# Optimization experiments

Measured on AMD Instinct MI355X. Metric: run time of the kernel, lower is better.

Reference implementation:

```python
import jax, jax.numpy as jnp
import numpy as np

N = 400000      # total tree nodes (forest batched together)
D = 256         # input feature dim
H = 128         # hidden_dim
C = 16          # num_classes (len(tag_dict))


def setup_inputs() -> dict:
    key = jax.random.key(0)
    ks = jax.random.split(key, 8)
    features = jax.random.normal(ks[0], (N, D), dtype=jnp.float32)
    # parent index per node; force parent[i] < i (topological order), root=0 self-parent
    raw = jax.random.randint(ks[1], (N,), 0, N)
    idx = jnp.arange(N)
    parent = jnp.where(idx == 0, 0, raw % jnp.maximum(idx, 1))
    init = lambda k, shp, fan: (jax.random.normal(k, shp, dtype=jnp.float32) / np.float32(np.sqrt(fan)))
    W1 = init(ks[2], (D, H), D); b1 = jnp.zeros((H,), jnp.float32)
    W2 = init(ks[3], (H, H), H); b2 = jnp.zeros((H,), jnp.float32)
    Wu = init(ks[4], (H, C), H); bu = jnp.zeros((C,), jnp.float32)
    We = init(ks[5], (2 * H, C * C), 2 * H); be = jnp.zeros((C * C,), jnp.float32)
    return {"features": features, "parent": parent,
            "W1": W1, "b1": b1, "W2": W2, "b2": b2,
            "Wu": Wu, "bu": bu, "We": We, "be": be}


def reference(features, parent, W1, b1, W2, b2, Wu, bu, We, be):
    # MLP feature extractor (num_layers=2, outputs hidden_dim)
    h = jax.nn.relu(features @ W1 + b1)          # [N, H]
    h = jax.nn.relu(h @ W2 + b2)                 # [N, H]
    # unary potentials per node
    unary = h @ Wu + bu                          # [N, C]
    # edge potentials per (parent, child) pair: cat(parent_hidden, child_hidden)
    edge_in = jnp.concatenate([h[parent], h], axis=1)   # [N, 2H] irregular gather
    edge = edge_in @ We + be                     # [N, C*C]
    # pack unary + edge potentials into a single output tensor
    return jnp.concatenate([unary, edge], axis=1)       # [N, C + C*C]
```

## Files before the change

### kernel.cpp

```cpp
#include <hip/hip_runtime.h>
#include <hip/hip_bf16.h>

typedef __bf16 bf16x8 __attribute__((ext_vector_type(8)));
typedef float  f32x4  __attribute__((ext_vector_type(4)));

#define MFMA16 __builtin_amdgcn_mfma_f32_16x16x32_bf16

__global__ void shuffle_weights(const float* __restrict__ W, __bf16* __restrict__ out,
                                int K, int Nw) {
    int tid = blockIdx.x * 256 + threadIdx.x;
    int NT = Nw >> 4;
    int total = (K >> 5) * NT * 64;
    if (tid >= total) return;
    int lane = tid & 63;
    int rest = tid >> 6;
    int nt = rest % NT;
    int kc = rest / NT;
    int q = lane >> 4;
    int n = nt * 16 + (lane & 15);
    const float* src = W + (size_t)(kc * 32 + q * 8) * Nw + n;
    __bf16* dst = out + (size_t)tid * 8;
#pragma unroll
    for (int j = 0; j < 8; ++j) dst[j] = (__bf16)src[(size_t)j * Nw];
}

__global__ __launch_bounds__(256) void phase1(
    const float* __restrict__ feat,
    const __bf16* __restrict__ W1s, const float* __restrict__ b1,
    const __bf16* __restrict__ W2s, const float* __restrict__ b2,
    __bf16* __restrict__ hbuf)
{
    __shared__ __bf16 h1s[128 * 136];
    const int lane = threadIdx.x & 63;
    const int wave = threadIdx.x >> 6;
    const int q    = lane >> 4;
    const int mr   = lane & 15;
    const long base = (long)blockIdx.x * 128 + wave * 32;

    const f32x4 fz = {0.f, 0.f, 0.f, 0.f};

    f32x4 acc[2][8];
#pragma unroll
    for (int mt = 0; mt < 2; ++mt)
#pragma unroll
        for (int nt = 0; nt < 8; ++nt) acc[mt][nt] = fz;

#pragma unroll
    for (int kc = 0; kc < 8; ++kc) {
        bf16x8 af[2];
#pragma unroll
        for (int mt = 0; mt < 2; ++mt) {
            const float* p = feat + (base + mt * 16 + mr) * 256 + kc * 32 + q * 8;
            f32x4 f0 = *(const f32x4*)p;
            f32x4 f1 = *(const f32x4*)(p + 4);
#pragma unroll
            for (int j = 0; j < 4; ++j) {
                af[mt][j]     = (__bf16)f0[j];
                af[mt][4 + j] = (__bf16)f1[j];
            }
        }
#pragma unroll
        for (int nt = 0; nt < 8; ++nt) {
            bf16x8 bf = *(const bf16x8*)(W1s + (size_t)((kc * 8 + nt) * 64 + lane) * 8);
            acc[0][nt] = MFMA16(af[0], bf, acc[0][nt], 0, 0, 0);
            acc[1][nt] = MFMA16(af[1], bf, acc[1][nt], 0, 0, 0);
        }
    }

#pragma unroll
    for (int mt = 0; mt < 2; ++mt)
#pragma unroll
        for (int nt = 0; nt < 8; ++nt) {
            int c = nt * 16 + mr;
            float bb = b1[c];
#pragma unroll
            for (int r = 0; r < 4; ++r) {
                float v = acc[mt][nt][r] + bb;
                v = v > 0.f ? v : 0.f;
                h1s[(wave * 32 + mt * 16 + q * 4 + r) * 136 + c] = (__bf16)v;
            }
        }
    __syncthreads();

    bf16x8 af2[2][4];
#pragma unroll
    for (int mt = 0; mt < 2; ++mt)
#pragma unroll
        for (int kc = 0; kc < 4; ++kc)
            af2[mt][kc] = *(const bf16x8*)&h1s[(wave * 32 + mt * 16 + mr) * 136 + kc * 32 + q * 8];

    f32x4 acc2[2][8];
#pragma unroll
    for (int mt = 0; mt < 2; ++mt)
#pragma unroll
        for (int nt = 0; nt < 8; ++nt) acc2[mt][nt] = fz;

#pragma unroll
    for (int kc = 0; kc < 4; ++kc)
#pragma unroll
        for (int nt = 0; nt < 8; ++nt) {
            bf16x8 bf = *(const bf16x8*)(W2s + (size_t)((kc * 8 + nt) * 64 + lane) * 8);
            acc2[0][nt] = MFMA16(af2[0][kc], bf, acc2[0][nt], 0, 0, 0);
            acc2[1][nt] = MFMA16(af2[1][kc], bf, acc2[1][nt], 0, 0, 0);
        }

#pragma unroll
    for (int mt = 0; mt < 2; ++mt)
#pragma unroll
        for (int nt = 0; nt < 8; ++nt) {
            int c = nt * 16 + mr;
            float bb = b2[c];
#pragma unroll
            for (int r = 0; r < 4; ++r) {
                float v = acc2[mt][nt][r] + bb;
                v = v > 0.f ? v : 0.f;
                hbuf[(base + mt * 16 + q * 4 + r) * 128 + c] = (__bf16)v;
            }
        }
}

__global__ __launch_bounds__(256) void phase2(
    const __bf16* __restrict__ hbuf, const int* __restrict__ parent,
    const __bf16* __restrict__ WeS, const float* __restrict__ be,
    const __bf16* __restrict__ WuS, const float* __restrict__ bu,
    float* __restrict__ out)
{
    const int lane = threadIdx.x & 63;
    const int q    = lane >> 4;
    const int mr   = lane & 15;
    const long base = (long)blockIdx.x * 128 + (threadIdx.x >> 6) * 32;

    const f32x4 fz = {0.f, 0.f, 0.f, 0.f};

    bf16x8 af[2][8];
#pragma unroll
    for (int mt = 0; mt < 2; ++mt) {
        long node = base + mt * 16 + mr;
        long par  = parent[node];
        const __bf16* hp = hbuf + par * 128;
        const __bf16* hn = hbuf + node * 128;
#pragma unroll
        for (int kc = 0; kc < 4; ++kc) {
            af[mt][kc]     = *(const bf16x8*)(hp + kc * 32 + q * 8);
            af[mt][kc + 4] = *(const bf16x8*)(hn + kc * 32 + q * 8);
        }
    }

    f32x4 accu[2];
    accu[0] = fz; accu[1] = fz;
#pragma unroll
    for (int kc = 0; kc < 4; ++kc) {
        bf16x8 bf = *(const bf16x8*)(WuS + (size_t)(kc * 64 + lane) * 8);
        accu[0] = MFMA16(af[0][kc + 4], bf, accu[0], 0, 0, 0);
        accu[1] = MFMA16(af[1][kc + 4], bf, accu[1], 0, 0, 0);
    }
    {
        float bb = bu[mr];
#pragma unroll
        for (int mt = 0; mt < 2; ++mt)
#pragma unroll
            for (int r = 0; r < 4; ++r)
                out[(base + mt * 16 + q * 4 + r) * 272 + mr] = accu[mt][r] + bb;
    }

#pragma unroll 1
    for (int nh = 0; nh < 2; ++nh) {
        f32x4 acc[2][8];
#pragma unroll
        for (int mt = 0; mt < 2; ++mt)
#pragma unroll
            for (int nt = 0; nt < 8; ++nt) acc[mt][nt] = fz;

#pragma unroll
        for (int kc = 0; kc < 8; ++kc)
#pragma unroll
            for (int nt = 0; nt < 8; ++nt) {
                bf16x8 bf = *(const bf16x8*)(WeS + (size_t)((kc * 16 + nh * 8 + nt) * 64 + lane) * 8);
                acc[0][nt] = MFMA16(af[0][kc], bf, acc[0][nt], 0, 0, 0);
                acc[1][nt] = MFMA16(af[1][kc], bf, acc[1][nt], 0, 0, 0);
            }

#pragma unroll
        for (int mt = 0; mt < 2; ++mt)
#pragma unroll
            for (int nt = 0; nt < 8; ++nt) {
                int c = nh * 128 + nt * 16 + mr;
                float bb = be[c];
#pragma unroll
                for (int r = 0; r < 4; ++r)
                    out[(base + mt * 16 + q * 4 + r) * 272 + 16 + c] = acc[mt][nt][r] + bb;
            }
    }
}

extern "C" void kernel_launch(void* const* d_in, const int* in_sizes, int n_in,
                              void* d_out, int out_size, void* d_ws, size_t ws_size,
                              hipStream_t stream) {
    const float* feat  = (const float*)d_in[0];
    const int*   parent = (const int*)d_in[1];
    const float* W1 = (const float*)d_in[2];
    const float* b1 = (const float*)d_in[3];
    const float* W2 = (const float*)d_in[4];
    const float* b2 = (const float*)d_in[5];
    const float* Wu = (const float*)d_in[6];
    const float* bu = (const float*)d_in[7];
    const float* We = (const float*)d_in[8];
    const float* be = (const float*)d_in[9];
    float* out = (float*)d_out;

    char* ws = (char*)d_ws;
    __bf16* W1s  = (__bf16*)(ws);
    __bf16* W2s  = (__bf16*)(ws + 65536);
    __bf16* WuS  = (__bf16*)(ws + 98304);
    __bf16* WeS  = (__bf16*)(ws + 102400);
    __bf16* hbuf = (__bf16*)(ws + 233472);

    shuffle_weights<<<16, 256, 0, stream>>>(W1, W1s, 256, 128);
    shuffle_weights<<<8,  256, 0, stream>>>(W2, W2s, 128, 128);
    shuffle_weights<<<1,  256, 0, stream>>>(Wu, WuS, 128, 16);
    shuffle_weights<<<32, 256, 0, stream>>>(We, WeS, 256, 256);

    const int nblocks = 400000 / 128;
    phase1<<<nblocks, 256, 0, stream>>>(feat, W1s, b1, W2s, b2, hbuf);
    phase2<<<nblocks, 256, 0, stream>>>(hbuf, parent, WeS, be, WuS, bu, out);
}
```

Measured before the change: 1.036 ms.

## Swap MFMA operands to produce transposed tiles enabling vectorized row-wise stores

The MFMA operands are swapped (weights as A, activations as B), so each lane holds four consecutive output columns of one row rather than four rows of one column. Epilogue stores become 16-byte float4 writes to the output and 8-byte bf16x4 writes to hbuf and LDS, replacing scattered scalar stores. Bias loads become float4. In phase2, activation fragments are reloaded per nh iteration instead of held in registers, which lowers register pressure but repeats the gather loads; the __syncthreads in phase1 is dropped, which is safe because each wave reads only its own LDS rows.

```diff
diff --git a/kernel.cpp b/kernel.cpp
--- a/kernel.cpp
+++ b/kernel.cpp
@@ -2,6 +2,7 @@
 #include <hip/hip_bf16.h>
 
 typedef __bf16 bf16x8 __attribute__((ext_vector_type(8)));
+typedef __bf16 bf16x4 __attribute__((ext_vector_type(4)));
 typedef float  f32x4  __attribute__((ext_vector_type(4)));
 
 #define MFMA16 __builtin_amdgcn_mfma_f32_16x16x32_bf16
@@ -39,11 +40,9 @@
 
     const f32x4 fz = {0.f, 0.f, 0.f, 0.f};
 
-    f32x4 acc[2][8];
-#pragma unroll
-    for (int mt = 0; mt < 2; ++mt)
-#pragma unroll
-        for (int nt = 0; nt < 8; ++nt) acc[mt][nt] = fz;
+    f32x4 acc[8][2];
+#pragma unroll
+    for (int ct = 0; ct < 8; ++ct) { acc[ct][0] = fz; acc[ct][1] = fz; }
 
 #pragma unroll
     for (int kc = 0; kc < 8; ++kc) {
@@ -60,27 +59,26 @@
             }
         }
 #pragma unroll
-        for (int nt = 0; nt < 8; ++nt) {
-            bf16x8 bf = *(const bf16x8*)(W1s + (size_t)((kc * 8 + nt) * 64 + lane) * 8);
-            acc[0][nt] = MFMA16(af[0], bf, acc[0][nt], 0, 0, 0);
-            acc[1][nt] = MFMA16(af[1], bf, acc[1][nt], 0, 0, 0);
+        for (int ct = 0; ct < 8; ++ct) {
+            bf16x8 bf = *(const bf16x8*)(W1s + (size_t)((kc * 8 + ct) * 64 + lane) * 8);
+            acc[ct][0] = MFMA16(bf, af[0], acc[ct][0], 0, 0, 0);
+            acc[ct][1] = MFMA16(bf, af[1], acc[ct][1], 0, 0, 0);
         }
     }
 
 #pragma unroll
     for (int mt = 0; mt < 2; ++mt)
 #pragma unroll
-        for (int nt = 0; nt < 8; ++nt) {
-            int c = nt * 16 + mr;
-            float bb = b1[c];
+        for (int ct = 0; ct < 8; ++ct) {
+            f32x4 bb = *(const f32x4*)(b1 + ct * 16 + q * 4);
+            bf16x4 v;
 #pragma unroll
             for (int r = 0; r < 4; ++r) {
-                float v = acc[mt][nt][r] + bb;
-                v = v > 0.f ? v : 0.f;
-                h1s[(wave * 32 + mt * 16 + q * 4 + r) * 136 + c] = (__bf16)v;
-            }
-        }
-    __syncthreads();
+                float x = acc[ct][mt][r] + bb[r];
+                v[r] = (__bf16)(x > 0.f ? x : 0.f);
+            }
+            *(bf16x4*)&h1s[(wave * 32 + mt * 16 + mr) * 136 + ct * 16 + q * 4] = v;
+        }
 
     bf16x8 af2[2][4];
 #pragma unroll
@@ -89,33 +87,31 @@
         for (int kc = 0; kc < 4; ++kc)
             af2[mt][kc] = *(const bf16x8*)&h1s[(wave * 32 + mt * 16 + mr) * 136 + kc * 32 + q * 8];
 
-    f32x4 acc2[2][8];
+    f32x4 acc2[8][2];
+#pragma unroll
+    for (int ct = 0; ct < 8; ++ct) { acc2[ct][0] = fz; acc2[ct][1] = fz; }
+
+#pragma unroll
+    for (int kc = 0; kc < 4; ++kc)
+#pragma unroll
+        for (int ct = 0; ct < 8; ++ct) {
+            bf16x8 bf = *(const bf16x8*)(W2s + (size_t)((kc * 8 + ct) * 64 + lane) * 8);
+            acc2[ct][0] = MFMA16(bf, af2[0][kc], acc2[ct][0], 0, 0, 0);
+            acc2[ct][1] = MFMA16(bf, af2[1][kc], acc2[ct][1], 0, 0, 0);
+        }
+
 #pragma unroll
     for (int mt = 0; mt < 2; ++mt)
 #pragma unroll
-        for (int nt = 0; nt < 8; ++nt) acc2[mt][nt] = fz;
-
-#pragma unroll
-    for (int kc = 0; kc < 4; ++kc)
-#pragma unroll
-        for (int nt = 0; nt < 8; ++nt) {
-            bf16x8 bf = *(const bf16x8*)(W2s + (size_t)((kc * 8 + nt) * 64 + lane) * 8);
-            acc2[0][nt] = MFMA16(af2[0][kc], bf, acc2[0][nt], 0, 0, 0);
-            acc2[1][nt] = MFMA16(af2[1][kc], bf, acc2[1][nt], 0, 0, 0);
-        }
-
-#pragma unroll
-    for (int mt = 0; mt < 2; ++mt)
-#pragma unroll
-        for (int nt = 0; nt < 8; ++nt) {
-            int c = nt * 16 + mr;
-            float bb = b2[c];
+        for (int ct = 0; ct < 8; ++ct) {
+            f32x4 bb = *(const f32x4*)(b2 + ct * 16 + q * 4);
+            bf16x4 v;
 #pragma unroll
             for (int r = 0; r < 4; ++r) {
-                float v = acc2[mt][nt][r] + bb;
-                v = v > 0.f ? v : 0.f;
-                hbuf[(base + mt * 16 + q * 4 + r) * 128 + c] = (__bf16)v;
-            }
+                float x = acc2[ct][mt][r] + bb[r];
+                v[r] = (__bf16)(x > 0.f ? x : 0.f);
+            }
+            *(bf16x4*)&hbuf[(base + mt * 16 + mr) * 128 + ct * 16 + q * 4] = v;
         }
 }
 
@@ -132,64 +128,55 @@
 
     const f32x4 fz = {0.f, 0.f, 0.f, 0.f};
 
-    bf16x8 af[2][8];
-#pragma unroll
-    for (int mt = 0; mt < 2; ++mt) {
-        long node = base + mt * 16 + mr;
-        long par  = parent[node];
-        const __bf16* hp = hbuf + par * 128;
-        const __bf16* hn = hbuf + node * 128;
+    const long n0 = base + mr;
+    const long n1 = base + 16 + mr;
+    const __bf16* hn0 = hbuf + n0 * 128;
+    const __bf16* hn1 = hbuf + n1 * 128;
+    const __bf16* hp0 = hbuf + (long)parent[n0] * 128;
+    const __bf16* hp1 = hbuf + (long)parent[n1] * 128;
+
+    {
+        f32x4 au0 = fz, au1 = fz;
 #pragma unroll
         for (int kc = 0; kc < 4; ++kc) {
-            af[mt][kc]     = *(const bf16x8*)(hp + kc * 32 + q * 8);
-            af[mt][kc + 4] = *(const bf16x8*)(hn + kc * 32 + q * 8);
-        }
-    }
-
-    f32x4 accu[2];
-    accu[0] = fz; accu[1] = fz;
-#pragma unroll
-    for (int kc = 0; kc < 4; ++kc) {
-        bf16x8 bf = *(const bf16x8*)(WuS + (size_t)(kc * 64 + lane) * 8);
-        accu[0] = MFMA16(af[0][kc + 4], bf, accu[0], 0, 0, 0);
-        accu[1] = MFMA16(af[1][kc + 4], bf, accu[1], 0, 0, 0);
-    }
-    {
-        float bb = bu[mr];
-#pragma unroll
-        for (int mt = 0; mt < 2; ++mt)
-#pragma unroll
-            for (int r = 0; r < 4; ++r)
-                out[(base + mt * 16 + q * 4 + r) * 272 + mr] = accu[mt][r] + bb;
+            bf16x8 a0 = *(const bf16x8*)(hn0 + kc * 32 + q * 8);
+            bf16x8 a1 = *(const bf16x8*)(hn1 + kc * 32 + q * 8);
+            bf16x8 bf = *(const bf16x8*)(WuS + (size_t)(kc * 64 + lane) * 8);
+            au0 = MFMA16(bf, a0, au0, 0, 0, 0);
+            au1 = MFMA16(bf, a1, au1, 0, 0, 0);
+        }
+        f32x4 bb = *(const f32x4*)(bu + q * 4);
+        *(f32x4*)&out[n0 * 272 + q * 4] = au0 + bb;
+        *(f32x4*)&out[n1 * 272 + q * 4] = au1 + bb;
     }
 
 #pragma unroll 1
     for (int nh = 0; nh < 2; ++nh) {
-        f32x4 acc[2][8];
-#pragma unroll
-        for (int mt = 0; mt < 2; ++mt)
-#pragma unroll
-            for (int nt = 0; nt < 8; ++nt) acc[mt][nt] = fz;
-
-#pragma unroll
-        for (int kc = 0; kc < 8; ++kc)
+        f32x4 acc[8][2];
+#pragma unroll
+        for (int nt = 0; nt < 8; ++nt) { acc[nt][0] = fz; acc[nt][1] = fz; }
+
+#pragma unroll
+        for (int kc = 0; kc < 8; ++kc) {
+            const __bf16* s0 = (kc < 4) ? (hp0 + kc * 32) : (hn0 + (kc - 4) * 32);
+            const __bf16* s1 = (kc < 4) ? (hp1 + kc * 32) : (hn1 + (kc - 4) * 32);
+            bf16x8 a0 = *(const bf16x8*)(s0 + q * 8);
+            bf16x8 a1 = *(const bf16x8*)(s1 + q * 8);
 #pragma unroll
             for (int nt = 0; nt < 8; ++nt) {
                 bf16x8 bf = *(const bf16x8*)(WeS + (size_t)((kc * 16 + nh * 8 + nt) * 64 + lane) * 8);
-                acc[0][nt] = MFMA16(af[0][kc], bf, acc[0][nt], 0, 0, 0);
-                acc[1][nt] = MFMA16(af[1][kc], bf, acc[1][nt], 0, 0, 0);
-            }
-
-#pragma unroll
-        for (int mt = 0; mt < 2; ++mt)
-#pragma unroll
-            for (int nt = 0; nt < 8; ++nt) {
-                int c = nh * 128 + nt * 16 + mr;
-                float bb = be[c];
-#pragma unroll
-                for (int r = 0; r < 4; ++r)
-                    out[(base + mt * 16 + q * 4 + r) * 272 + 16 + c] = acc[mt][nt][r] + bb;
-            }
+                acc[nt][0] = MFMA16(bf, a0, acc[nt][0], 0, 0, 0);
+                acc[nt][1] = MFMA16(bf, a1, acc[nt][1], 0, 0, 0);
+            }
+        }
+
+#pragma unroll
+        for (int nt = 0; nt < 8; ++nt) {
+            int c0 = nh * 128 + nt * 16 + q * 4;
+            f32x4 bb = *(const f32x4*)(be + c0);
+            *(f32x4*)&out[n0 * 272 + 16 + c0] = acc[nt][0] + bb;
+            *(f32x4*)&out[n1 * 272 + 16 + c0] = acc[nt][1] + bb;
+        }
     }
 }
 
```

After: 989.9 us. 4.4% less time.
